# Performance work log

Measured on AMD Instinct MI355X. Metric: run time of the kernel, lower is better.

## Reference

```python
import jax, jax.numpy as jnp
import numpy as np

N_HEADS = 8
N_GROUPS = 32
EPS = 1e-5


def setup_inputs() -> dict:
    key = jax.random.key(0)
    ks = jax.random.split(key, 3)
    b, c, h, w = 8, 512, 32, 32
    x = jax.random.normal(ks[0], (b, c, h, w), dtype=jnp.float32)
    gamma = jnp.ones((c,), jnp.float32)
    beta = jnp.zeros((c,), jnp.float32)
    w_qkv = jax.random.normal(ks[1], (3 * c, c), jnp.float32) * (1.0 / np.sqrt(c))
    b_qkv = jnp.zeros((3 * c,), jnp.float32)
    w_proj = jax.random.normal(ks[2], (c, c), jnp.float32) * (1.0 / np.sqrt(c))
    b_proj = jnp.zeros((c,), jnp.float32)
    return {"x": x, "gamma": gamma, "beta": beta, "w_qkv": w_qkv,
            "b_qkv": b_qkv, "w_proj": w_proj, "b_proj": b_proj}


def _group_norm(x, gamma, beta):
    # x: [b, c, T]; GroupNorm over (c//G, T) per group, computed in fp32
    b, c, t = x.shape
    xg = x.reshape(b, N_GROUPS, c // N_GROUPS, t).astype(jnp.float32)
    mean = xg.mean(axis=(2, 3), keepdims=True)
    var = xg.var(axis=(2, 3), keepdims=True)
    xg = (xg - mean) * jax.lax.rsqrt(var + EPS)
    xn = xg.reshape(b, c, t).astype(x.dtype)
    return xn * gamma[None, :, None] + beta[None, :, None]


def reference(x, gamma, beta, w_qkv, b_qkv, w_proj, b_proj):
    b, c, *spatial = x.shape
    t = int(np.prod(spatial))
    xf = x.reshape(b, c, t)
    h = _group_norm(xf, gamma, beta)
    # 1x1 conv == channel matmul
    qkv = jnp.einsum('oc,bct->bot', w_qkv, h) + b_qkv[None, :, None]  # [b, 3c, t]
    ch = c // N_HEADS
    qkv = qkv.reshape(b * N_HEADS, 3 * ch, t)
    q, k, v = qkv[:, :ch], qkv[:, ch:2 * ch], qkv[:, 2 * ch:]
    scale = 1.0 / np.sqrt(np.sqrt(ch))
    weight = jnp.einsum('bct,bcs->bts', q * scale, k * scale)
    weight = jax.nn.softmax(weight.astype(jnp.float32), axis=-1).astype(weight.dtype)
    a = jnp.einsum('bts,bcs->bct', weight, v)  # [b*H, ch, t]
    a = a.reshape(b, c, t)
    h = jnp.einsum('oc,bct->bot', w_proj, a) + b_proj[None, :, None]
    return (xf + h).reshape(b, c, *spatial)
```

## Files before the change

### kernel.cpp

```cpp
#include <hip/hip_runtime.h>
#include <hip/hip_bf16.h>
#include <math.h>

#define BATCH 8
#define CDIM 512
#define TDIM 1024
#define NHD 8

typedef __attribute__((ext_vector_type(8))) _Float16 f16x8;
typedef __attribute__((ext_vector_type(4))) float floatx4;

#define QSCALE 0.18033688011112042f

static __device__ __forceinline__ unsigned short f2h(float f) {
    _Float16 h = (_Float16)f;
    return *reinterpret_cast<unsigned short*>(&h);
}
static __device__ __forceinline__ void async_load16(const unsigned short* gsrc,
                                                    unsigned short* ldst) {
    __builtin_amdgcn_global_load_lds(
        (const __attribute__((address_space(1))) void*)gsrc,
        (__attribute__((address_space(3))) void*)ldst, 16, 0, 0);
}

__global__ __launch_bounds__(256) void prep_kernel(
    const float* __restrict__ x, const float* __restrict__ gamma,
    const float* __restrict__ beta, const float* __restrict__ w_qkv,
    const float* __restrict__ w_proj, unsigned short* __restrict__ h_t,
    unsigned short* __restrict__ wq, unsigned short* __restrict__ wp) {
    int tid = threadIdx.x;
    if (blockIdx.x >= 256) {
        int i = (blockIdx.x - 256) * 256 + tid;
        const int nA = 1536 * 512 / 4;
        const float* s;
        unsigned short* d;
        int j;
        if (i < nA) { s = w_qkv; d = wq; j = i; }
        else        { s = w_proj; d = wp; j = i - nA; }
        float4 v = ((const float4*)s)[j];
        ushort4 o;
        o.x = f2h(v.x); o.y = f2h(v.y); o.z = f2h(v.z); o.w = f2h(v.w);
        ((ushort4*)d)[j] = o;
        return;
    }
    int bg = blockIdx.x;
    int b = bg >> 5, g = bg & 31;
    const float* xp = x + ((size_t)(b * CDIM + g * 16)) * TDIM;

    float s = 0.f, ss = 0.f;
    for (int r = 0; r < 16; ++r) {
        float4 v = ((const float4*)xp)[r * 256 + tid];
        s  += v.x + v.y + v.z + v.w;
        ss += v.x * v.x + v.y * v.y + v.z * v.z + v.w * v.w;
    }
    for (int off = 32; off > 0; off >>= 1) {
        s  += __shfl_down(s, off, 64);
        ss += __shfl_down(ss, off, 64);
    }
    __shared__ float rs[4], rss[4], stat[2];
    int wave = tid >> 6;
    if ((tid & 63) == 0) { rs[wave] = s; rss[wave] = ss; }
    __syncthreads();
    if (tid == 0) {
        float S  = rs[0] + rs[1] + rs[2] + rs[3];
        float SS = rss[0] + rss[1] + rss[2] + rss[3];
        float mean = S * (1.f / 16384.f);
        float var  = SS * (1.f / 16384.f) - mean * mean;
        stat[0] = mean;
        stat[1] = rsqrtf(var + 1e-5f);
    }
    __syncthreads();
    float mean = stat[0], rstd = stat[1];

    int cpair = tid & 7, trow = tid >> 3;
    int c0 = g * 16 + cpair * 2;
    float g0 = gamma[c0] * rstd,  g1 = gamma[c0 + 1] * rstd;
    float b0 = beta[c0] - mean * g0, b1 = beta[c0 + 1] - mean * g1;
    const float* x0 = x + ((size_t)(b * CDIM + c0)) * TDIM;
    const float* x1 = x0 + TDIM;
    unsigned int* hp = (unsigned int*)h_t + (size_t)b * TDIM * 256 + g * 8 + cpair;
    for (int p = 0; p < 32; ++p) {
        int t = p * 32 + trow;
        float v0 = x0[t] * g0 + b0;
        float v1 = x1[t] * g1 + b1;
        hp[(size_t)t * 256] = (unsigned)f2h(v0) | ((unsigned)f2h(v1) << 16);
    }
}

__global__ __launch_bounds__(256) void mfma_gemm(
    const unsigned short* __restrict__ Wb,
    const unsigned short* __restrict__ Xt,
    const float* __restrict__ bias,
    int M, int K, int mode,
    unsigned short* __restrict__ q_t,
    unsigned short* __restrict__ k_t,
    unsigned short* __restrict__ v,
    const float* __restrict__ resid,
    float* __restrict__ outp) {
    __shared__ __align__(16) unsigned short As[2 * 128 * 32];
    __shared__ __align__(16) unsigned short Bs[2 * 128 * 32];

    int tid = threadIdx.x;
    int n0 = blockIdx.x * 128, m0 = blockIdx.y * 128, bb = blockIdx.z;
    const unsigned short* Xp = Xt + (size_t)bb * TDIM * K;

    int lane = tid & 63, w = tid >> 6;
    int l15 = lane & 15, quad = lane >> 4;
    int wm = w >> 1, wn = w & 1;

    const unsigned short* aSrc[4];
    const unsigned short* bSrc[4];
    unsigned short* aDst[4];
    unsigned short* bDst[4];
#pragma unroll
    for (int c = 0; c < 4; ++c) {
        int slot = w * 256 + c * 64 + lane;
        int panel = slot >> 9, row = (slot >> 2) & 127, g4 = slot & 3;
        aSrc[c] = Wb + (size_t)(m0 + row) * K + panel * 32 + g4 * 8;
        bSrc[c] = Xp + (size_t)(n0 + row) * K + panel * 32 + g4 * 8;
        aDst[c] = &As[(w * 256 + c * 64) * 8];
        bDst[c] = &Bs[(w * 256 + c * 64) * 8];
    }

    floatx4 acc[4][4];
#pragma unroll
    for (int i = 0; i < 4; ++i)
#pragma unroll
        for (int j = 0; j < 4; ++j) acc[i][j] = (floatx4){0.f, 0.f, 0.f, 0.f};

    for (int k0 = 0; k0 < K; k0 += 64) {
#pragma unroll
        for (int c = 0; c < 4; ++c) {
            async_load16(aSrc[c] + k0, aDst[c]);
            async_load16(bSrc[c] + k0, bDst[c]);
        }
        __syncthreads();
#pragma unroll
        for (int kc = 0; kc < 2; ++kc) {
            f16x8 af[4], bfr[4];
#pragma unroll
            for (int mi = 0; mi < 4; ++mi)
                af[mi] = *(const f16x8*)&As[(kc * 128 + wm * 64 + mi * 16 + l15) * 32 + quad * 8];
#pragma unroll
            for (int ni = 0; ni < 4; ++ni)
                bfr[ni] = *(const f16x8*)&Bs[(kc * 128 + wn * 64 + ni * 16 + l15) * 32 + quad * 8];
#pragma unroll
            for (int mi = 0; mi < 4; ++mi)
#pragma unroll
                for (int ni = 0; ni < 4; ++ni)
                    acc[mi][ni] = __builtin_amdgcn_mfma_f32_16x16x32_f16(
                        af[mi], bfr[ni], acc[mi][ni], 0, 0, 0);
        }
        __syncthreads();
    }

    int b8 = bb * NHD;
#pragma unroll
    for (int mi = 0; mi < 4; ++mi) {
        int mBase = m0 + wm * 64 + mi * 16 + quad * 4;
#pragma unroll
        for (int ni = 0; ni < 4; ++ni) {
            floatx4 a = acc[mi][ni];
            int n = n0 + wn * 64 + ni * 16 + l15;
            if (mode == 0) {
                int chunk = mBase >> 6;
                int hd = chunk / 3, part = chunk % 3;
                int cB = mBase & 63;
                if (part == 0) {
                    ushort4 pk;
                    pk.x = f2h((a[0] + bias[mBase + 0]) * QSCALE);
                    pk.y = f2h((a[1] + bias[mBase + 1]) * QSCALE);
                    pk.z = f2h((a[2] + bias[mBase + 2]) * QSCALE);
                    pk.w = f2h((a[3] + bias[mBase + 3]) * QSCALE);
                    *(ushort4*)&q_t[((size_t)(b8 + hd) * TDIM + n) * 64 + cB] = pk;
                } else if (part == 1) {
                    ushort4 pk;
                    pk.x = f2h(a[0] + bias[mBase + 0]);
                    pk.y = f2h(a[1] + bias[mBase + 1]);
                    pk.z = f2h(a[2] + bias[mBase + 2]);
                    pk.w = f2h(a[3] + bias[mBase + 3]);
                    *(ushort4*)&k_t[((size_t)(b8 + hd) * TDIM + n) * 64 + cB] = pk;
                } else {
#pragma unroll
                    for (int r = 0; r < 4; ++r)
                        v[((size_t)(b8 + hd) * 64 + cB + r) * TDIM + n] =
                            f2h(a[r] + bias[mBase + r]);
                }
            } else {
                size_t base = ((size_t)bb * CDIM + mBase) * TDIM + n;
#pragma unroll
                for (int r = 0; r < 4; ++r)
                    outp[base + (size_t)r * TDIM] =
                        a[r] + bias[mBase + r] + resid[base + (size_t)r * TDIM];
            }
        }
    }
}

__global__ __launch_bounds__(256, 1) void attn_kernel(
    const unsigned short* __restrict__ q_t,
    const unsigned short* __restrict__ k_t,
    const unsigned short* __restrict__ v,
    unsigned short* __restrict__ a_t) {
    __shared__ __align__(16) unsigned short Qs[256 * 64];
    __shared__ __align__(16) unsigned short Kb[2][64 * 64];
    __shared__ __align__(16) unsigned short Vb[2][64 * 64];

    int tid = threadIdx.x;
    int q0 = blockIdx.x * 256;
    int bh = blockIdx.y;
    int lane = tid & 63, w = tid >> 6;
    int l15 = lane & 15, quad = lane >> 4;
    int l7 = l15 & 7;

    const unsigned short* Qp = q_t + (size_t)bh * TDIM * 64;
    const unsigned short* Kp = k_t + (size_t)bh * TDIM * 64;
    const unsigned short* Vp = v + (size_t)bh * 64 * TDIM;

#pragma unroll
    for (int c = 0; c < 8; ++c) {
        int s_ = w * 512 + c * 64 + lane;
        int r = s_ >> 3, gs = s_ & 7, g = gs ^ (r & 7);
        async_load16(Qp + (size_t)(q0 + r) * 64 + g * 8, &Qs[(w * 512 + c * 64) * 8]);
    }

    int kofs[2], vofs[2];
    unsigned short* kdst[2];
    unsigned short* vdst[2];
#pragma unroll
    for (int c = 0; c < 2; ++c) {
        int s_ = w * 128 + c * 64 + lane;
        int m = s_ >> 3, gs = s_ & 7, g = gs ^ (m & 7);
        int mi = m >> 4, qq = (m >> 2) & 3, rr = m & 3;
        int pm = (mi & 1) * 32 + qq * 8 + (mi >> 1) * 4 + rr;
        kofs[c] = pm * 64 + g * 8;
        vofs[c] = m * TDIM + g * 8;
        kdst[c] = &Kb[0][(w * 128 + c * 64) * 8];
        vdst[c] = &Vb[0][(w * 128 + c * 64) * 8];
    }
    const int bufstep = 64 * 64;

#pragma unroll
    for (int c = 0; c < 2; ++c) {
        async_load16(Kp + kofs[c], kdst[c]);
        async_load16(Vp + vofs[c], vdst[c]);
    }
    __syncthreads();

    f16x8 qf[4][2];
#pragma unroll
    for (int f = 0; f < 4; ++f)
#pragma unroll
        for (int ch = 0; ch < 2; ++ch)
            qf[f][ch] = *(const f16x8*)&Qs[(w * 64 + f * 16 + l15) * 64 +
                                           ((ch * 4 + quad) ^ l7) * 8];

    floatx4 o_acc[4][4];
#pragma unroll
    for (int i = 0; i < 4; ++i)
#pragma unroll
        for (int j = 0; j < 4; ++j) o_acc[i][j] = (floatx4){0.f, 0.f, 0.f, 0.f};
    float m_run[4] = {-INFINITY, -INFINITY, -INFINITY, -INFINITY};
    float l_run[4] = {0.f, 0.f, 0.f, 0.f};

    for (int it = 0; it < 16; ++it) {
        int cur = it & 1;
        if (it < 15) {
            int s0n = (it + 1) * 64;
#pragma unroll
            for (int c = 0; c < 2; ++c) {
                async_load16(Kp + (size_t)s0n * 64 + kofs[c], kdst[c] + (cur ^ 1) * bufstep);
                async_load16(Vp + s0n + vofs[c], vdst[c] + (cur ^ 1) * bufstep);
            }
        }
        f16x8 kf[4][2], vf[4][2];
#pragma unroll
        for (int mi = 0; mi < 4; ++mi)
#pragma unroll
            for (int ch = 0; ch < 2; ++ch) {
                int off = (mi * 16 + l15) * 64 + ((ch * 4 + quad) ^ l7) * 8;
                kf[mi][ch] = *(const f16x8*)&Kb[cur][off];
                vf[mi][ch] = *(const f16x8*)&Vb[cur][off];
            }

        f16x8 pf[4][2];
#pragma unroll
        for (int f = 0; f < 4; ++f) {
            floatx4 sT[4];
#pragma unroll
            for (int mi = 0; mi < 4; ++mi) {
                floatx4 z = (floatx4){0.f, 0.f, 0.f, 0.f};
                z = __builtin_amdgcn_mfma_f32_16x16x32_f16(kf[mi][0], qf[f][0], z, 0, 0, 0);
                z = __builtin_amdgcn_mfma_f32_16x16x32_f16(kf[mi][1], qf[f][1], z, 0, 0, 0);
                sT[mi] = z;
            }
            float mx = sT[0][0];
#pragma unroll
            for (int mi = 0; mi < 4; ++mi)
#pragma unroll
                for (int r = 0; r < 4; ++r) mx = fmaxf(mx, sT[mi][r]);
            mx = fmaxf(mx, __shfl_xor(mx, 16));
            mx = fmaxf(mx, __shfl_xor(mx, 32));
            float mn = fmaxf(m_run[f], mx);
            float alpha = __builtin_amdgcn_exp2f(m_run[f] - mn);
            float sum = 0.f;
#pragma unroll
            for (int mi = 0; mi < 4; ++mi)
#pragma unroll
                for (int r = 0; r < 4; ++r) {
                    float p = __builtin_amdgcn_exp2f(sT[mi][r] - mn);
                    sT[mi][r] = p;
                    sum += p;
                }
            sum += __shfl_xor(sum, 16);
            sum += __shfl_xor(sum, 32);
            l_run[f] = l_run[f] * alpha + sum;
            m_run[f] = mn;
#pragma unroll
            for (int ci = 0; ci < 4; ++ci) {
                o_acc[ci][f][0] *= alpha; o_acc[ci][f][1] *= alpha;
                o_acc[ci][f][2] *= alpha; o_acc[ci][f][3] *= alpha;
            }
#pragma unroll
            for (int kb = 0; kb < 2; ++kb) {
                pf[f][kb][0] = (_Float16)sT[kb][0];
                pf[f][kb][1] = (_Float16)sT[kb][1];
                pf[f][kb][2] = (_Float16)sT[kb][2];
                pf[f][kb][3] = (_Float16)sT[kb][3];
                pf[f][kb][4] = (_Float16)sT[kb + 2][0];
                pf[f][kb][5] = (_Float16)sT[kb + 2][1];
                pf[f][kb][6] = (_Float16)sT[kb + 2][2];
                pf[f][kb][7] = (_Float16)sT[kb + 2][3];
            }
        }
#pragma unroll
        for (int ci = 0; ci < 4; ++ci)
#pragma unroll
            for (int f = 0; f < 4; ++f)
#pragma unroll
                for (int kb = 0; kb < 2; ++kb)
                    o_acc[ci][f] = __builtin_amdgcn_mfma_f32_16x16x32_f16(
                        vf[ci][kb], pf[f][kb], o_acc[ci][f], 0, 0, 0);
        __syncthreads();
    }

    int b = bh >> 3, hd = bh & 7;
#pragma unroll
    for (int f = 0; f < 4; ++f) {
        float linv = 1.f / l_run[f];
        int t = q0 + w * 64 + f * 16 + l15;
        size_t rowb = ((size_t)b * TDIM + t) * CDIM + hd * 64 + quad * 4;
#pragma unroll
        for (int ci = 0; ci < 4; ++ci) {
            ushort4 pk;
            pk.x = f2h(o_acc[ci][f][0] * linv);
            pk.y = f2h(o_acc[ci][f][1] * linv);
            pk.z = f2h(o_acc[ci][f][2] * linv);
            pk.w = f2h(o_acc[ci][f][3] * linv);
            *(ushort4*)&a_t[rowb + ci * 16] = pk;
        }
    }
}

extern "C" void kernel_launch(void* const* d_in, const int* in_sizes, int n_in,
                              void* d_out, int out_size, void* d_ws, size_t ws_size,
                              hipStream_t stream) {
    (void)in_sizes; (void)n_in; (void)out_size; (void)ws_size;
    const float* x      = (const float*)d_in[0];
    const float* gamma  = (const float*)d_in[1];
    const float* beta   = (const float*)d_in[2];
    const float* w_qkv  = (const float*)d_in[3];
    const float* b_qkv  = (const float*)d_in[4];
    const float* w_proj = (const float*)d_in[5];
    const float* b_proj = (const float*)d_in[6];
    float* out = (float*)d_out;

    unsigned short* wq  = (unsigned short*)d_ws;
    unsigned short* wp  = wq + 1536 * 512;
    unsigned short* h_t = wp + 512 * 512;
    unsigned short* q_t = h_t + (size_t)BATCH * TDIM * CDIM;
    unsigned short* k_t = q_t + (size_t)64 * TDIM * 64;
    unsigned short* vv  = k_t + (size_t)64 * TDIM * 64;
    unsigned short* a_t = vv + (size_t)64 * TDIM * 64;

    prep_kernel<<<1280, 256, 0, stream>>>(x, gamma, beta, w_qkv, w_proj, h_t, wq, wp);

    mfma_gemm<<<dim3(8, 12, BATCH), 256, 0, stream>>>(
        wq, h_t, b_qkv, 1536, 512, 0, q_t, k_t, vv, nullptr, nullptr);

    attn_kernel<<<dim3(4, 64), 256, 0, stream>>>(q_t, k_t, vv, a_t);

    mfma_gemm<<<dim3(8, 4, BATCH), 256, 0, stream>>>(
        wp, a_t, b_proj, 512, 512, 1, nullptr, nullptr, nullptr, x, out);
}
```

Baseline: 178.9 us.

## Halve attention query tile to double grid and allow two blocks per CU

The attention kernel now processes 128 queries per block instead of 256, and the grid changes to (64 heads, 8 query tiles) with launch bounds allowing two blocks per CU. Q fragments are loaded directly from global memory into registers rather than staged through shared memory, and the V fragment loads are moved after the QK MFMAs. The goal is more waves in flight and better CU coverage to hide latency. In exchange, each K/V tile is loaded twice as often overall, and the Q global loads are not swizzled.

```diff
diff --git a/kernel.cpp b/kernel.cpp
--- a/kernel.cpp
+++ b/kernel.cpp
@@ -197,18 +197,17 @@
     }
 }
 
-__global__ __launch_bounds__(256, 1) void attn_kernel(
+__global__ __launch_bounds__(256, 2) void attn_kernel(
     const unsigned short* __restrict__ q_t,
     const unsigned short* __restrict__ k_t,
     const unsigned short* __restrict__ v,
     unsigned short* __restrict__ a_t) {
-    __shared__ __align__(16) unsigned short Qs[256 * 64];
     __shared__ __align__(16) unsigned short Kb[2][64 * 64];
     __shared__ __align__(16) unsigned short Vb[2][64 * 64];
 
     int tid = threadIdx.x;
-    int q0 = blockIdx.x * 256;
-    int bh = blockIdx.y;
+    int bh = blockIdx.x;
+    int q0 = blockIdx.y * 128;
     int lane = tid & 63, w = tid >> 6;
     int l15 = lane & 15, quad = lane >> 4;
     int l7 = l15 & 7;
@@ -216,13 +215,6 @@
     const unsigned short* Qp = q_t + (size_t)bh * TDIM * 64;
     const unsigned short* Kp = k_t + (size_t)bh * TDIM * 64;
     const unsigned short* Vp = v + (size_t)bh * 64 * TDIM;
-
-#pragma unroll
-    for (int c = 0; c < 8; ++c) {
-        int s_ = w * 512 + c * 64 + lane;
-        int r = s_ >> 3, gs = s_ & 7, g = gs ^ (r & 7);
-        async_load16(Qp + (size_t)(q0 + r) * 64 + g * 8, &Qs[(w * 512 + c * 64) * 8]);
-    }
 
     int kofs[2], vofs[2];
     unsigned short* kdst[2];
@@ -245,23 +237,24 @@
         async_load16(Kp + kofs[c], kdst[c]);
         async_load16(Vp + vofs[c], vdst[c]);
     }
+
+    f16x8 qf[2][2];
+#pragma unroll
+    for (int f = 0; f < 2; ++f)
+#pragma unroll
+        for (int ch = 0; ch < 2; ++ch)
+            qf[f][ch] = *(const f16x8*)(Qp + (size_t)(q0 + w * 32 + f * 16 + l15) * 64 +
+                                        (ch * 4 + quad) * 8);
+
+    floatx4 o_acc[4][2];
+#pragma unroll
+    for (int i = 0; i < 4; ++i)
+#pragma unroll
+        for (int j = 0; j < 2; ++j) o_acc[i][j] = (floatx4){0.f, 0.f, 0.f, 0.f};
+    float m_run[2] = {-INFINITY, -INFINITY};
+    float l_run[2] = {0.f, 0.f};
+
     __syncthreads();
-
-    f16x8 qf[4][2];
-#pragma unroll
-    for (int f = 0; f < 4; ++f)
-#pragma unroll
-        for (int ch = 0; ch < 2; ++ch)
-            qf[f][ch] = *(const f16x8*)&Qs[(w * 64 + f * 16 + l15) * 64 +
-                                           ((ch * 4 + quad) ^ l7) * 8];
-
-    floatx4 o_acc[4][4];
-#pragma unroll
-    for (int i = 0; i < 4; ++i)
-#pragma unroll
-        for (int j = 0; j < 4; ++j) o_acc[i][j] = (floatx4){0.f, 0.f, 0.f, 0.f};
-    float m_run[4] = {-INFINITY, -INFINITY, -INFINITY, -INFINITY};
-    float l_run[4] = {0.f, 0.f, 0.f, 0.f};
 
     for (int it = 0; it < 16; ++it) {
         int cur = it & 1;
@@ -273,32 +266,41 @@
                 async_load16(Vp + s0n + vofs[c], vdst[c] + (cur ^ 1) * bufstep);
             }
         }
-        f16x8 kf[4][2], vf[4][2];
+        f16x8 kf[4][2];
 #pragma unroll
         for (int mi = 0; mi < 4; ++mi)
 #pragma unroll
-            for (int ch = 0; ch < 2; ++ch) {
-                int off = (mi * 16 + l15) * 64 + ((ch * 4 + quad) ^ l7) * 8;
-                kf[mi][ch] = *(const f16x8*)&Kb[cur][off];
-                vf[mi][ch] = *(const f16x8*)&Vb[cur][off];
-            }
-
-        f16x8 pf[4][2];
-#pragma unroll
-        for (int f = 0; f < 4; ++f) {
-            floatx4 sT[4];
+            for (int ch = 0; ch < 2; ++ch)
+                kf[mi][ch] = *(const f16x8*)&Kb[cur][(mi * 16 + l15) * 64 +
+                                                    ((ch * 4 + quad) ^ l7) * 8];
+
+        floatx4 sT[2][4];
+#pragma unroll
+        for (int f = 0; f < 2; ++f)
 #pragma unroll
             for (int mi = 0; mi < 4; ++mi) {
                 floatx4 z = (floatx4){0.f, 0.f, 0.f, 0.f};
                 z = __builtin_amdgcn_mfma_f32_16x16x32_f16(kf[mi][0], qf[f][0], z, 0, 0, 0);
                 z = __builtin_amdgcn_mfma_f32_16x16x32_f16(kf[mi][1], qf[f][1], z, 0, 0, 0);
-                sT[mi] = z;
-            }
-            float mx = sT[0][0];
+                sT[f][mi] = z;
+            }
+
+        f16x8 vf[4][2];
+#pragma unroll
+        for (int ci = 0; ci < 4; ++ci)
+#pragma unroll
+            for (int ch = 0; ch < 2; ++ch)
+                vf[ci][ch] = *(const f16x8*)&Vb[cur][(ci * 16 + l15) * 64 +
+                                                    ((ch * 4 + quad) ^ l7) * 8];
+
+        f16x8 pf[2][2];
+#pragma unroll
+        for (int f = 0; f < 2; ++f) {
+            float mx = sT[f][0][0];
 #pragma unroll
             for (int mi = 0; mi < 4; ++mi)
 #pragma unroll
-                for (int r = 0; r < 4; ++r) mx = fmaxf(mx, sT[mi][r]);
+                for (int r = 0; r < 4; ++r) mx = fmaxf(mx, sT[f][mi][r]);
             mx = fmaxf(mx, __shfl_xor(mx, 16));
             mx = fmaxf(mx, __shfl_xor(mx, 32));
             float mn = fmaxf(m_run[f], mx);
@@ -308,8 +310,8 @@
             for (int mi = 0; mi < 4; ++mi)
 #pragma unroll
                 for (int r = 0; r < 4; ++r) {
-                    float p = __builtin_amdgcn_exp2f(sT[mi][r] - mn);
-                    sT[mi][r] = p;
+                    float p = __builtin_amdgcn_exp2f(sT[f][mi][r] - mn);
+                    sT[f][mi][r] = p;
                     sum += p;
                 }
             sum += __shfl_xor(sum, 16);
@@ -323,20 +325,21 @@
             }
 #pragma unroll
             for (int kb = 0; kb < 2; ++kb) {
-                pf[f][kb][0] = (_Float16)sT[kb][0];
-                pf[f][kb][1] = (_Float16)sT[kb][1];
-                pf[f][kb][2] = (_Float16)sT[kb][2];
-                pf[f][kb][3] = (_Float16)sT[kb][3];
-                pf[f][kb][4] = (_Float16)sT[kb + 2][0];
-                pf[f][kb][5] = (_Float16)sT[kb + 2][1];
-                pf[f][kb][6] = (_Float16)sT[kb + 2][2];
-                pf[f][kb][7] = (_Float16)sT[kb + 2][3];
-            }
-        }
+                pf[f][kb][0] = (_Float16)sT[f][kb][0];
+                pf[f][kb][1] = (_Float16)sT[f][kb][1];
+                pf[f][kb][2] = (_Float16)sT[f][kb][2];
+                pf[f][kb][3] = (_Float16)sT[f][kb][3];
+                pf[f][kb][4] = (_Float16)sT[f][kb + 2][0];
+                pf[f][kb][5] = (_Float16)sT[f][kb + 2][1];
+                pf[f][kb][6] = (_Float16)sT[f][kb + 2][2];
+                pf[f][kb][7] = (_Float16)sT[f][kb + 2][3];
+            }
+        }
+
 #pragma unroll
         for (int ci = 0; ci < 4; ++ci)
 #pragma unroll
-            for (int f = 0; f < 4; ++f)
+            for (int f = 0; f < 2; ++f)
 #pragma unroll
                 for (int kb = 0; kb < 2; ++kb)
                     o_acc[ci][f] = __builtin_amdgcn_mfma_f32_16x16x32_f16(
@@ -346,9 +349,9 @@
 
     int b = bh >> 3, hd = bh & 7;
 #pragma unroll
-    for (int f = 0; f < 4; ++f) {
+    for (int f = 0; f < 2; ++f) {
         float linv = 1.f / l_run[f];
-        int t = q0 + w * 64 + f * 16 + l15;
+        int t = q0 + w * 32 + f * 16 + l15;
         size_t rowb = ((size_t)b * TDIM + t) * CDIM + hd * 64 + quad * 4;
 #pragma unroll
         for (int ci = 0; ci < 4; ++ci) {
@@ -388,7 +391,7 @@
     mfma_gemm<<<dim3(8, 12, BATCH), 256, 0, stream>>>(
         wq, h_t, b_qkv, 1536, 512, 0, q_t, k_t, vv, nullptr, nullptr);
 
-    attn_kernel<<<dim3(4, 64), 256, 0, stream>>>(q_t, k_t, vv, a_t);
+    attn_kernel<<<dim3(64, 8), 256, 0, stream>>>(q_t, k_t, vv, a_t);
 
     mfma_gemm<<<dim3(8, 4, BATCH), 256, 0, stream>>>(
         wp, a_t, b_proj, 512, 512, 1, nullptr, nullptr, nullptr, x, out);
```

New measurement: 165.9 us. 1.08x faster.
